# Kernel tuning notes

Hardware: AMD Instinct MI355X
Metric: run time of the kernel (lower is better)

## Reference

```python
import math
import jax, jax.numpy as jnp
from jax import lax
import numpy as np

N, C, H, W = 32, 256, 56, 56

def setup_inputs() -> dict:
    key = jax.random.key(0)
    k = jax.random.split(key, 5)
    return {
        "x": jax.random.normal(k[0], (N, C, H, W), dtype=jnp.float32),
        "p1_w": jax.random.normal(k[1], (H, W, C, 1), dtype=jnp.float32) * 0.1,
        "conv_w": jax.random.normal(k[2], (C, C // 2, 3, 3), dtype=jnp.float32) * 0.05,
        "p4_w": jax.random.normal(k[3], (1, C, C), dtype=jnp.float32) * 0.1,
        "p5_w": jax.random.normal(k[4], (C, 1), dtype=jnp.float32) * 0.1,
    }

def reference(x, p1_w, conv_w, p4_w, p5_w):
    n, c, h, w = x.shape
    inv_sqrt_c = 1.0 / math.sqrt(c)
    # t_1: einsum 'abcd,cdef->abef' -> [n, c, c, 1] -> [n, c, c]
    t1 = jnp.einsum('nchw,hwef->ncef', x, p1_w)[..., 0]
    # t_3: grouped 3x3 conv, groups=2, no bias -> [n, c, h, w]
    t3 = lax.conv_general_dilated(
        x, conv_w, window_strides=(1, 1), padding=((1, 1), (1, 1)),
        dimension_numbers=('NCHW', 'OIHW', 'NCHW'), feature_group_count=2)
    # t_4: broadcast elementwise scale [1,c,c] * [n,c,c]
    t4 = p4_w * t1
    # t_5: [n,c,c] @ [c,1] -> [n,c]
    t5 = jnp.einsum('nab,bo->nao', t4, p5_w)[..., 0]
    # t_6: bmm(t4 [n,c,c], t3 [n,c,hw]) / sqrt(c) -> [n,c,h,w]
    t6 = (jnp.einsum('nab,nbs->nas', t4, t3.reshape(n, c, h * w))
          .reshape(n, c, h, w)) * inv_sqrt_c
    # t_7: bmm(t5 [n,1,c], x [n,c,hw]) / sqrt(c) -> [n,h,w]
    t7 = (jnp.einsum('nc,ncs->ns', t5, x.reshape(n, c, h * w))
          .reshape(n, h, w)) * inv_sqrt_c
    # t_8: broadcast add [n,1,h,w] + [n,c,h,w]
    return t7[:, None, :, :] + t6
```

## Files before the change

kernel.cpp:

```cpp
#include <hip/hip_runtime.h>

#define HWB   3136
#define HWPAD 3200
#define SPAD  3364

typedef __attribute__((ext_vector_type(8))) short bf16x8;
typedef __attribute__((ext_vector_type(4))) float f32x4;

__device__ __forceinline__ unsigned short f2bf(float f) {
    unsigned u = __float_as_uint(f);
    unsigned r = (u + 0x7fffu + ((u >> 16) & 1u)) >> 16;
    return (unsigned short)r;
}
__device__ __forceinline__ float bf2f(unsigned short h) {
    return __uint_as_float(((unsigned)h) << 16);
}
__device__ __forceinline__ void gl_lds16(const void* g, void* l) {
    __builtin_amdgcn_global_load_lds(
        (const __attribute__((address_space(1))) void*)g,
        (__attribute__((address_space(3))) void*)l, 16, 0, 0);
}

__global__ __launch_bounds__(256) void k_prep(
    const float* __restrict__ x, unsigned short* __restrict__ xc,
    unsigned short* __restrict__ xp)
{
    __shared__ unsigned short tile[32][33];
    const int n = blockIdx.z, c0 = blockIdx.y * 32, s0 = blockIdx.x * 32;
    const int lx = threadIdx.x & 31, ly = threadIdx.x >> 5;
    const float* xb = x + ((size_t)(n * 256 + c0)) * HWB + s0;
    unsigned short* xcb = xc + ((size_t)(n * 256 + c0)) * HWB + s0;
#pragma unroll
    for (int it = 0; it < 4; ++it) {
        int lc = ly + it * 8;
        unsigned short b = f2bf(xb[(size_t)lc * HWB + lx]);
        tile[lc][lx] = b;
        xcb[(size_t)lc * HWB + lx] = b;
    }
    __syncthreads();
    unsigned short* ob = xp + (size_t)n * SPAD * 256 + c0;
#pragma unroll
    for (int it = 0; it < 4; ++it) {
        int ls = ly + it * 8;
        int s = s0 + ls;
        int sp = s + 2 * (s / 56) + 59;
        ob[(size_t)sp * 256 + lx] = tile[lx][ls];
    }
}

__global__ __launch_bounds__(256) void k_prep_p1t(
    const float* __restrict__ p1, unsigned short* __restrict__ p1t)
{
    __shared__ unsigned short tile[32][33];
    const int e0 = blockIdx.y * 32, h0 = blockIdx.x * 32;
    const int lx = threadIdx.x & 31, ly = threadIdx.x >> 5;
#pragma unroll
    for (int it = 0; it < 4; ++it) {
        int lh = ly + it * 8;
        tile[lh][lx] = f2bf(p1[(size_t)(h0 + lh) * 256 + e0 + lx]);
    }
    __syncthreads();
#pragma unroll
    for (int it = 0; it < 4; ++it) {
        int le = ly + it * 8;
        p1t[(size_t)(e0 + le) * HWB + h0 + lx] = tile[lx][le];
    }
}

__global__ __launch_bounds__(256) void k_prep_w(
    const float* __restrict__ w, unsigned short* __restrict__ wp,
    unsigned short* __restrict__ xp)
{
    const int o = blockIdx.x, t = threadIdx.x;
#pragma unroll
    for (int k = t; k < 1152; k += 256) {
        int tap = k >> 7, ci = k & 127;
        wp[(size_t)o * 1152 + k] = f2bf(w[(size_t)o * 1152 + ci * 9 + tap]);
    }
    if (o < 32) {
        unsigned short* xpn = xp + (size_t)o * SPAD * 256;
        for (int sp = t; sp < SPAD; sp += 256) {
            int y = sp / 58, xcol = sp - y * 58;
            if (y == 0 || y == 57 || xcol == 0 || xcol == 57) {
                ushort4 z4 = {0, 0, 0, 0};
#pragma unroll
                for (int k = 0; k < 64; ++k)
                    *(ushort4*)&xpn[(size_t)sp * 256 + k * 4] = z4;
            }
        }
    }
}

__global__ __launch_bounds__(256) void k_conv(
    const unsigned short* __restrict__ xp, const unsigned short* __restrict__ wp,
    unsigned short* __restrict__ t3cl)
{
    __shared__ short As[2][128 * 64];
    __shared__ short Bs[2][128 * 64];
    const int tid = threadIdx.x;
    const int orig = blockIdx.x;
    const int wgid = (orig & 7) * 200 + (orig >> 3);
    const int ng = wgid / 25;
    const int tileS = (wgid - ng * 25) * 128;
    const int n = ng >> 1, g = ng & 1;
    const int wave = tid >> 6, lane = tid & 63;
    const int wm = (wave >> 1) * 64, wn = (wave & 1) * 64;

    const int rl = tid >> 3, q = tid & 7;
    const int swq = (q ^ (rl & 7)) * 8;

    const unsigned short* xpn = xp + (size_t)n * SPAD * 256 + g * 128 + swq;
    const unsigned short* arow[4];
    const unsigned short* brow[4];
#pragma unroll
    for (int p = 0; p < 4; ++p) {
        int s = tileS + p * 32 + rl;
        int sc = s < HWB ? s : HWB - 1;
        int sp = sc + 2 * (sc / 56) + 59;
        arow[p] = xpn + (size_t)sp * 256;
        brow[p] = wp + (size_t)(g * 128 + p * 32 + rl) * 1152 + swq;
    }

    f32x4 acc[4][4] = {};
    const int frow = lane & 15, quad = lane >> 4, sw = frow & 7;
    int rofA[4], rofB[4];
#pragma unroll
    for (int i = 0; i < 4; ++i) {
        rofA[i] = (wm + i * 16 + frow) * 64;
        rofB[i] = (wn + i * 16 + frow) * 64;
    }
    const int ldst = (tid >> 3) * 64 + (tid & 7) * 8;

    {
        const int shift0 = (-59) * 256;
#pragma unroll
        for (int p = 0; p < 4; ++p) {
            gl_lds16(arow[p] + shift0, &As[0][p * 2048 + ldst]);
            gl_lds16(brow[p], &Bs[0][p * 2048 + ldst]);
        }
    }
    __syncthreads();

    int cur = 0;
#pragma unroll
    for (int t = 0; t < 18; ++t) {
        if (t < 17) {
            const int tn = t + 1;
            const int tap = tn >> 1;
            const int shift = ((tap / 3 - 1) * 58 + (tap % 3 - 1)) * 256 + (tn & 1) * 64;
#pragma unroll
            for (int p = 0; p < 4; ++p) {
                gl_lds16(arow[p] + shift, &As[cur ^ 1][p * 2048 + ldst]);
                gl_lds16(brow[p] + tn * 64, &Bs[cur ^ 1][p * 2048 + ldst]);
            }
        }
        const short* Ab = As[cur];
        const short* Bb = Bs[cur];
#pragma unroll
        for (int h = 0; h < 2; ++h) {
            bf16x8 af[4], bfr[4];
#pragma unroll
            for (int i = 0; i < 4; ++i)
                af[i] = *(const bf16x8*)&Ab[rofA[i] + ((h * 4 + quad) ^ sw) * 8];
#pragma unroll
            for (int j = 0; j < 4; ++j)
                bfr[j] = *(const bf16x8*)&Bb[rofB[j] + ((h * 4 + quad) ^ sw) * 8];
#pragma unroll
            for (int i = 0; i < 4; ++i)
#pragma unroll
                for (int j = 0; j < 4; ++j)
                    acc[i][j] = __builtin_amdgcn_mfma_f32_16x16x32_bf16(af[i], bfr[j], acc[i][j], 0, 0, 0);
        }
        __syncthreads();
        cur ^= 1;
    }
    unsigned short* ob = t3cl + (size_t)n * HWPAD * 256 + g * 128;
#pragma unroll
    for (int i = 0; i < 4; ++i)
#pragma unroll
        for (int r = 0; r < 4; ++r) {
            int s = tileS + wm + i * 16 + (lane >> 4) * 4 + r;
            int c = wn + (lane & 15);
#pragma unroll
            for (int j = 0; j < 4; ++j) {
                float v = (s < HWB) ? acc[i][j][r] : 0.f;
                ob[(size_t)s * 256 + c + j * 16] = f2bf(v);
            }
        }
}

__global__ __launch_bounds__(256) void k_gemm1(
    const unsigned short* __restrict__ xc, const unsigned short* __restrict__ p1t,
    float* __restrict__ part)
{
    __shared__ short As[2][128 * 64];
    __shared__ short Bs[2][128 * 64];
    const int tid = threadIdx.x;
    const int orig = blockIdx.x;
    const int wgid = (orig & 7) * 64 + (orig >> 3);
    const int z = wgid >> 7;
    const int rem = wgid & 127;
    const int tileM = (rem >> 1) * 128;
    const int tileN = (rem & 1) * 128;
    const int kbase = z ? (832 + (z - 1) * 768) : 0;
    const int nk = z ? 12 : 13;
    const int wave = tid >> 6, lane = tid & 63;
    const int wm = (wave >> 1) * 64, wn = (wave & 1) * 64;

    const int rl = tid >> 3, q = tid & 7;
    const int swq = (q ^ (rl & 7)) * 8;
    const unsigned short* asrc = xc + (size_t)(tileM + rl) * HWB + kbase + swq;
    const unsigned short* bsrc = p1t + (size_t)(tileN + rl) * HWB + kbase + swq;

    f32x4 acc[4][4] = {};
    const int frow = lane & 15, quad = lane >> 4, sw = frow & 7;
    const int ldst = rl * 64 + q * 8;

#pragma unroll
    for (int p = 0; p < 4; ++p) {
        gl_lds16(asrc + (size_t)(p * 32) * HWB, &As[0][p * 2048 + ldst]);
        gl_lds16(bsrc + (size_t)(p * 32) * HWB, &Bs[0][p * 2048 + ldst]);
    }
    __syncthreads();

    int cur = 0;
    for (int i2 = 0; i2 < nk; ++i2) {
        if (i2 + 1 < nk) {
            const int kn = (i2 + 1) * 64;
#pragma unroll
            for (int p = 0; p < 4; ++p) {
                gl_lds16(asrc + (size_t)(p * 32) * HWB + kn, &As[cur ^ 1][p * 2048 + ldst]);
                gl_lds16(bsrc + (size_t)(p * 32) * HWB + kn, &Bs[cur ^ 1][p * 2048 + ldst]);
            }
        }
        const short* Ab = As[cur];
        const short* Bb = Bs[cur];
#pragma unroll
        for (int h = 0; h < 2; ++h) {
            bf16x8 af[4], bfr[4];
#pragma unroll
            for (int i = 0; i < 4; ++i)
                af[i] = *(const bf16x8*)&Ab[(wm + i * 16 + frow) * 64 + ((h * 4 + quad) ^ sw) * 8];
#pragma unroll
            for (int j = 0; j < 4; ++j)
                bfr[j] = *(const bf16x8*)&Bb[(wn + j * 16 + frow) * 64 + ((h * 4 + quad) ^ sw) * 8];
#pragma unroll
            for (int i = 0; i < 4; ++i)
#pragma unroll
                for (int j = 0; j < 4; ++j)
                    acc[i][j] = __builtin_amdgcn_mfma_f32_16x16x32_bf16(af[i], bfr[j], acc[i][j], 0, 0, 0);
        }
        __syncthreads();
        cur ^= 1;
    }
    float* ob = part + (size_t)z * 8192 * 256;
#pragma unroll
    for (int j = 0; j < 4; ++j) {
        const int e = tileN + wn + j * 16 + (lane & 15);
#pragma unroll
        for (int i = 0; i < 4; ++i)
#pragma unroll
            for (int r = 0; r < 4; ++r) {
                int m = tileM + wm + i * 16 + (lane >> 4) * 4 + r;
                ob[(size_t)m * 256 + e] = acc[i][j][r];
            }
    }
}

__global__ __launch_bounds__(256) void k_t4scale(
    const float* __restrict__ part, const float* __restrict__ p4,
    const float* __restrict__ p5, unsigned short* __restrict__ t4h,
    float* __restrict__ t5)
{
    const int row = blockIdx.x * 4 + (threadIdx.x >> 6);
    const int lane = threadIdx.x & 63;
    const size_t off = (size_t)row * 256 + lane * 4;
    const size_t slab = (size_t)8192 * 256;
    float4 a0 = *(const float4*)&part[off];
    float4 a1 = *(const float4*)&part[off + slab];
    float4 a2 = *(const float4*)&part[off + 2 * slab];
    float4 a3 = *(const float4*)&part[off + 3 * slab];
    float4 a;
    a.x = (a0.x + a1.x) + (a2.x + a3.x);
    a.y = (a0.y + a1.y) + (a2.y + a3.y);
    a.z = (a0.z + a1.z) + (a2.z + a3.z);
    a.w = (a0.w + a1.w) + (a2.w + a3.w);
    float4 sc = *(const float4*)&p4[(size_t)(row & 255) * 256 + lane * 4];
    float4 pv = *(const float4*)&p5[lane * 4];
    float v0 = a.x * sc.x, v1 = a.y * sc.y, v2 = a.z * sc.z, v3 = a.w * sc.w;
    ushort4 o;
    o.x = f2bf(v0); o.y = f2bf(v1); o.z = f2bf(v2); o.w = f2bf(v3);
    *(ushort4*)&t4h[(size_t)row * 256 + lane * 4] = o;
    float sum = v0 * pv.x + v1 * pv.y + v2 * pv.z + v3 * pv.w;
#pragma unroll
    for (int offd = 32; offd > 0; offd >>= 1) sum += __shfl_down(sum, offd);
    if (lane == 0) t5[row] = sum;
}

__global__ __launch_bounds__(256) void k_t7(
    const unsigned short* __restrict__ xp, const float* __restrict__ t5,
    float* __restrict__ t7)
{
    const int n = blockIdx.y;
    const int wave = threadIdx.x >> 6, lane = threadIdx.x & 63;
    float4 w = *(const float4*)&t5[n * 256 + lane * 4];
    const int s0 = blockIdx.x * 16 + wave * 4;
#pragma unroll
    for (int qq = 0; qq < 4; ++qq) {
        const int s = s0 + qq;
        const int sp = s + 2 * (s / 56) + 59;
        ushort4 a = *(const ushort4*)&xp[((size_t)n * SPAD + sp) * 256 + lane * 4];
        float sum = bf2f(a.x) * w.x + bf2f(a.y) * w.y + bf2f(a.z) * w.z + bf2f(a.w) * w.w;
#pragma unroll
        for (int off = 32; off > 0; off >>= 1) sum += __shfl_down(sum, off);
        if (lane == 0) t7[n * HWB + s] = sum * 0.0625f;
    }
}

__global__ __launch_bounds__(256) void k_bmm(
    const unsigned short* __restrict__ t4h, const unsigned short* __restrict__ t3cl,
    const float* __restrict__ t7, float* __restrict__ out)
{
    __shared__ short As[2][128 * 64];
    __shared__ short Bs[2][128 * 64];
    const int tid = threadIdx.x;
    const int orig = blockIdx.x;
    const int wgid = (orig & 7) * 200 + (orig >> 3);
    const int n = wgid / 50;
    const int rem = wgid - n * 50;
    const int tileA = (rem / 25) * 128;
    const int tileS = (rem % 25) * 128;
    const int wave = tid >> 6, lane = tid & 63;
    const int wm = (wave >> 1) * 64, wn = (wave & 1) * 64;

    const int rl = tid >> 3, q = tid & 7;
    const int swq = (q ^ (rl & 7)) * 8;
    const unsigned short* asrc = t4h + ((size_t)n * 256 + tileA + rl) * 256 + swq;
    const unsigned short* bsrc = t3cl + ((size_t)n * HWPAD + tileS + rl) * 256 + swq;

    f32x4 acc[4][4] = {};
    const int frow = lane & 15, quad = lane >> 4, sw = frow & 7;
    const int ldst = rl * 64 + q * 8;

#pragma unroll
    for (int p = 0; p < 4; ++p) {
        gl_lds16(asrc + (size_t)(p * 32) * 256, &As[0][p * 2048 + ldst]);
        gl_lds16(bsrc + (size_t)(p * 32) * 256, &Bs[0][p * 2048 + ldst]);
    }
    __syncthreads();

    int cur = 0;
#pragma unroll
    for (int k0 = 0; k0 < 256; k0 += 64) {
        if (k0 < 192) {
            const int kn = k0 + 64;
#pragma unroll
            for (int p = 0; p < 4; ++p) {
                gl_lds16(asrc + (size_t)(p * 32) * 256 + kn, &As[cur ^ 1][p * 2048 + ldst]);
                gl_lds16(bsrc + (size_t)(p * 32) * 256 + kn, &Bs[cur ^ 1][p * 2048 + ldst]);
            }
        }
        const short* Ab = As[cur];
        const short* Bb = Bs[cur];
#pragma unroll
        for (int h = 0; h < 2; ++h) {
            bf16x8 af[4], bfr[4];
#pragma unroll
            for (int i = 0; i < 4; ++i)
                af[i] = *(const bf16x8*)&Ab[(wm + i * 16 + frow) * 64 + ((h * 4 + quad) ^ sw) * 8];
#pragma unroll
            for (int j = 0; j < 4; ++j)
                bfr[j] = *(const bf16x8*)&Bb[(wn + j * 16 + frow) * 64 + ((h * 4 + quad) ^ sw) * 8];
#pragma unroll
            for (int i = 0; i < 4; ++i)
#pragma unroll
                for (int j = 0; j < 4; ++j)
                    acc[i][j] = __builtin_amdgcn_mfma_f32_16x16x32_bf16(af[i], bfr[j], acc[i][j], 0, 0, 0);
        }
        __syncthreads();
        cur ^= 1;
    }
    const float* t7n = t7 + (size_t)n * HWB;
    float* ob = out + (size_t)n * 256 * HWB;
#pragma unroll
    for (int j = 0; j < 4; ++j) {
        int s = tileS + wn + j * 16 + (lane & 15);
        bool vsx = s < HWB;
        float t7v = vsx ? t7n[s] : 0.f;
        if (!vsx) continue;
#pragma unroll
        for (int i = 0; i < 4; ++i)
#pragma unroll
            for (int r = 0; r < 4; ++r) {
                int a = tileA + wm + i * 16 + (lane >> 4) * 4 + r;
                ob[(size_t)a * HWB + s] = acc[i][j][r] * 0.0625f + t7v;
            }
    }
}

extern "C" void kernel_launch(void* const* d_in, const int* in_sizes, int n_in,
                              void* d_out, int out_size, void* d_ws, size_t ws_size,
                              hipStream_t stream) {
    const float* x  = (const float*)d_in[0];
    const float* p1 = (const float*)d_in[1];
    const float* cw = (const float*)d_in[2];
    const float* p4 = (const float*)d_in[3];
    const float* p5 = (const float*)d_in[4];

    char* w = (char*)d_ws;
    unsigned short* xp    = (unsigned short*)w;  w += (size_t)32 * SPAD * 256 * 2;
    unsigned short* t3cl  = (unsigned short*)w;  w += (size_t)32 * HWPAD * 256 * 2;
    unsigned short* p1t   = (unsigned short*)w;  w += (size_t)256 * HWB * 2;
    unsigned short* wpack = (unsigned short*)w;  w += (size_t)256 * 1152 * 2;
    unsigned short* t4h   = (unsigned short*)w;  w += (size_t)8192 * 256 * 2;
    float* t5             = (float*)w;           w += (size_t)8192 * 4;
    float* t7             = (float*)w;           w += (size_t)32 * HWB * 4;

    char* o = (char*)d_out;
    unsigned short* xc = (unsigned short*)o;
    float* part        = (float*)(o + (size_t)32 * 256 * HWB * 2);
    float* out = (float*)d_out;

    k_prep    <<<dim3(98, 8, 32), 256, 0, stream>>>(x, xc, xp);
    k_prep_p1t<<<dim3(98, 8),     256, 0, stream>>>(p1, p1t);
    k_prep_w  <<<dim3(256),       256, 0, stream>>>(cw, wpack, xp);
    k_conv    <<<dim3(1600),      256, 0, stream>>>(xp, wpack, t3cl);
    k_gemm1   <<<dim3(512),       256, 0, stream>>>(xc, p1t, part);
    k_t4scale <<<dim3(2048),      256, 0, stream>>>(part, p4, p5, t4h, t5);
    k_t7      <<<dim3(196, 32),   256, 0, stream>>>(xp, t5, t7);
    k_bmm     <<<dim3(1600),      256, 0, stream>>>(t4h, t3cl, t7, out);
}
```

Before: 368.5 us.

## Vectorize prep transpose, split halo zeroing, and rework t7 reduction over channels

The prep kernel now handles 64x64 tiles with float4 loads and 16-byte bf16 stores for both the channel-major and padded channel-last copies. Zeroing of the padding border moves from the weight-prep kernel into a dedicated kernel that writes only the halo rows and columns. The t7 kernel now reads the contiguous channel-major xc copy, with each thread accumulating 8 spatial outputs over 32 channels, and combines partial sums with atomics into a buffer memset to zero beforehand. This replaces per-pixel wave reductions with coalesced loads, at the cost of an extra memset and atomic traffic, and the atomics make summation order nondeterministic.

Result: no change. 369.4 us (+0.2%).

```diff
diff --git a/kernel.cpp b/kernel.cpp
--- a/kernel.cpp
+++ b/kernel.cpp
@@ -25,27 +25,57 @@
     const float* __restrict__ x, unsigned short* __restrict__ xc,
     unsigned short* __restrict__ xp)
 {
-    __shared__ unsigned short tile[32][33];
-    const int n = blockIdx.z, c0 = blockIdx.y * 32, s0 = blockIdx.x * 32;
-    const int lx = threadIdx.x & 31, ly = threadIdx.x >> 5;
-    const float* xb = x + ((size_t)(n * 256 + c0)) * HWB + s0;
-    unsigned short* xcb = xc + ((size_t)(n * 256 + c0)) * HWB + s0;
-#pragma unroll
-    for (int it = 0; it < 4; ++it) {
-        int lc = ly + it * 8;
-        unsigned short b = f2bf(xb[(size_t)lc * HWB + lx]);
-        tile[lc][lx] = b;
-        xcb[(size_t)lc * HWB + lx] = b;
-    }
-    __syncthreads();
-    unsigned short* ob = xp + (size_t)n * SPAD * 256 + c0;
-#pragma unroll
-    for (int it = 0; it < 4; ++it) {
-        int ls = ly + it * 8;
-        int s = s0 + ls;
-        int sp = s + 2 * (s / 56) + 59;
-        ob[(size_t)sp * 256 + lx] = tile[lx][ls];
-    }
+    __shared__ short tile[64 * 66];
+    const int n = blockIdx.z, c0 = blockIdx.y * 64, s0 = blockIdx.x * 64;
+    const int t = threadIdx.x;
+    const int cl = t >> 2;
+    const int sq = (t & 3) * 16;
+
+    const float* src = x + ((size_t)(n * 256 + c0 + cl)) * HWB + s0 + sq;
+    unsigned short bf[16];
+#pragma unroll
+    for (int j = 0; j < 4; ++j) {
+        float4 v = *(const float4*)(src + j * 4);
+        bf[j * 4 + 0] = f2bf(v.x); bf[j * 4 + 1] = f2bf(v.y);
+        bf[j * 4 + 2] = f2bf(v.z); bf[j * 4 + 3] = f2bf(v.w);
+    }
+    unsigned short* xcb = xc + ((size_t)(n * 256 + c0 + cl)) * HWB + s0 + sq;
+    *(bf16x8*)xcb = *(const bf16x8*)&bf[0];
+    *(bf16x8*)(xcb + 8) = *(const bf16x8*)&bf[8];
+#pragma unroll
+    for (int k = 0; k < 16; ++k)
+        tile[(sq + k) * 66 + cl] = (short)bf[k];
+    __syncthreads();
+    const int r = t >> 2;
+    const int cq = (t & 3) * 16;
+    unsigned short ob[16];
+#pragma unroll
+    for (int j = 0; j < 8; ++j) {
+        unsigned w = *(const unsigned*)&tile[r * 66 + cq + 2 * j];
+        ob[2 * j] = (unsigned short)w;
+        ob[2 * j + 1] = (unsigned short)(w >> 16);
+    }
+    const int s = s0 + r;
+    const int sp = s + 2 * (s / 56) + 59;
+    unsigned short* dst = xp + ((size_t)n * SPAD + sp) * 256 + c0 + cq;
+    *(bf16x8*)dst = *(const bf16x8*)&ob[0];
+    *(bf16x8*)(dst + 8) = *(const bf16x8*)&ob[8];
+}
+
+__global__ __launch_bounds__(256) void k_zero(
+    unsigned short* __restrict__ xp)
+{
+    const int n = blockIdx.y;
+    const int idx = blockIdx.x * 256 + threadIdx.x;
+    if (idx >= 228 * 32) return;
+    const int i = idx >> 5, ch = idx & 31;
+    int sp;
+    if (i < 58)       sp = i;
+    else if (i < 116) sp = 3306 + (i - 58);
+    else if (i < 172) sp = (i - 115) * 58;
+    else              sp = (i - 171) * 58 + 57;
+    bf16x8 z = {};
+    *(bf16x8*)&xp[((size_t)n * SPAD + sp) * 256 + ch * 8] = z;
 }
 
 __global__ __launch_bounds__(256) void k_prep_p1t(
@@ -68,26 +98,13 @@
 }
 
 __global__ __launch_bounds__(256) void k_prep_w(
-    const float* __restrict__ w, unsigned short* __restrict__ wp,
-    unsigned short* __restrict__ xp)
+    const float* __restrict__ w, unsigned short* __restrict__ wp)
 {
     const int o = blockIdx.x, t = threadIdx.x;
 #pragma unroll
     for (int k = t; k < 1152; k += 256) {
         int tap = k >> 7, ci = k & 127;
         wp[(size_t)o * 1152 + k] = f2bf(w[(size_t)o * 1152 + ci * 9 + tap]);
-    }
-    if (o < 32) {
-        unsigned short* xpn = xp + (size_t)o * SPAD * 256;
-        for (int sp = t; sp < SPAD; sp += 256) {
-            int y = sp / 58, xcol = sp - y * 58;
-            if (y == 0 || y == 57 || xcol == 0 || xcol == 57) {
-                ushort4 z4 = {0, 0, 0, 0};
-#pragma unroll
-                for (int k = 0; k < 64; ++k)
-                    *(ushort4*)&xpn[(size_t)sp * 256 + k * 4] = z4;
-            }
-        }
     }
 }
 
@@ -298,23 +315,30 @@
 }
 
 __global__ __launch_bounds__(256) void k_t7(
-    const unsigned short* __restrict__ xp, const float* __restrict__ t5,
+    const unsigned short* __restrict__ xc, const float* __restrict__ t5,
     float* __restrict__ t7)
 {
-    const int n = blockIdx.y;
-    const int wave = threadIdx.x >> 6, lane = threadIdx.x & 63;
-    float4 w = *(const float4*)&t5[n * 256 + lane * 4];
-    const int s0 = blockIdx.x * 16 + wave * 4;
-#pragma unroll
-    for (int qq = 0; qq < 4; ++qq) {
-        const int s = s0 + qq;
-        const int sp = s + 2 * (s / 56) + 59;
-        ushort4 a = *(const ushort4*)&xp[((size_t)n * SPAD + sp) * 256 + lane * 4];
-        float sum = bf2f(a.x) * w.x + bf2f(a.y) * w.y + bf2f(a.z) * w.z + bf2f(a.w) * w.w;
-#pragma unroll
-        for (int off = 32; off > 0; off >>= 1) sum += __shfl_down(sum, off);
-        if (lane == 0) t7[n * HWB + s] = sum * 0.0625f;
-    }
+    const int n = blockIdx.z;
+    const int c0 = blockIdx.y * 32;
+    const int s0 = blockIdx.x * 1568;
+    __shared__ float wv[32];
+    const int t = threadIdx.x;
+    if (t < 32) wv[t] = t5[n * 256 + c0 + t];
+    __syncthreads();
+    if (t >= 196) return;
+    const unsigned short* base = xc + ((size_t)(n * 256 + c0)) * HWB + s0 + t * 8;
+    float acc[8] = {};
+    for (int c = 0; c < 32; ++c) {
+        bf16x8 v = *(const bf16x8*)(base + (size_t)c * HWB);
+        float w = wv[c];
+#pragma unroll
+        for (int j = 0; j < 8; ++j)
+            acc[j] += w * bf2f((unsigned short)v[j]);
+    }
+    float* dst = t7 + (size_t)n * HWB + s0 + t * 8;
+#pragma unroll
+    for (int j = 0; j < 8; ++j)
+        atomicAdd(&dst[j], acc[j] * 0.0625f);
 }
 
 __global__ __launch_bounds__(256) void k_bmm(
@@ -421,12 +445,14 @@
     float* part        = (float*)(o + (size_t)32 * 256 * HWB * 2);
     float* out = (float*)d_out;
 
-    k_prep    <<<dim3(98, 8, 32), 256, 0, stream>>>(x, xc, xp);
+    hipMemsetAsync(t7, 0, (size_t)32 * HWB * 4, stream);
+    k_prep    <<<dim3(49, 4, 32), 256, 0, stream>>>(x, xc, xp);
+    k_zero    <<<dim3(29, 32),    256, 0, stream>>>(xp);
     k_prep_p1t<<<dim3(98, 8),     256, 0, stream>>>(p1, p1t);
-    k_prep_w  <<<dim3(256),       256, 0, stream>>>(cw, wpack, xp);
+    k_prep_w  <<<dim3(256),       256, 0, stream>>>(cw, wpack);
     k_conv    <<<dim3(1600),      256, 0, stream>>>(xp, wpack, t3cl);
     k_gemm1   <<<dim3(512),       256, 0, stream>>>(xc, p1t, part);
     k_t4scale <<<dim3(2048),      256, 0, stream>>>(part, p4, p5, t4h, t5);
-    k_t7      <<<dim3(196, 32),   256, 0, stream>>>(xp, t5, t7);
+    k_t7      <<<dim3(2, 8, 32),  256, 0, stream>>>(xc, t5, t7);
     k_bmm     <<<dim3(1600),      256, 0, stream>>>(t4h, t3cl, t7, out);
 }
```
